# Optimization experiments

Measured on AMD Instinct MI355X. Metric: run time of the kernel, lower is better.

## Reference

```python
import jax, jax.numpy as jnp
import numpy as np

HIDDEN = 768
NUM_HEADS = 12
HEAD_SIZE = HIDDEN // NUM_HEADS
LN_EPS = 1e-5


def setup_inputs() -> dict:
    key = jax.random.key(0)
    ks = jax.random.split(key, 10)
    B, S, H = 2, 4096, HIDDEN
    std = 1.0 / np.sqrt(H)
    inp = {
        "hidden_states": jax.random.normal(ks[0], (B, S, H), dtype=jnp.float32),
        "attention_mask": jnp.ones((B, S), dtype=jnp.float32),
        "Wq": jax.random.normal(ks[1], (H, H), dtype=jnp.float32) * std,
        "bq": jnp.zeros((H,), dtype=jnp.float32),
        "Wk": jax.random.normal(ks[2], (H, H), dtype=jnp.float32) * std,
        "bk": jnp.zeros((H,), dtype=jnp.float32),
        "Wv": jax.random.normal(ks[3], (H, H), dtype=jnp.float32) * std,
        "bv": jnp.zeros((H,), dtype=jnp.float32),
        "Wo": jax.random.normal(ks[4], (H, H), dtype=jnp.float32) * std,
        "bo": jnp.zeros((H,), dtype=jnp.float32),
        "ln_gamma": jnp.ones((H,), dtype=jnp.float32),
        "ln_beta": jnp.zeros((H,), dtype=jnp.float32),
    }
    return inp


def _split_heads(x):
    # [B, S, H] -> [B, nH, S, hd]
    B, S, _ = x.shape
    return x.reshape(B, S, NUM_HEADS, HEAD_SIZE).transpose(0, 2, 1, 3)


def reference(hidden_states, attention_mask, Wq, bq, Wk, bk, Wv, bv, Wo, bo, ln_gamma, ln_beta):
    # QKV projections (torch Linear: x @ W.T + b; here W is stored as [in, out])
    q = _split_heads(hidden_states @ Wq + bq)
    k = _split_heads(hidden_states @ Wk + bk)
    v = _split_heads(hidden_states @ Wv + bv)

    scores = jnp.einsum("bhqd,bhkd->bhqk", q, k) / jnp.sqrt(jnp.float32(HEAD_SIZE))
    # additive mask: (1 - mask) * -10000, broadcast over heads and query positions
    scores = scores + (1.0 - attention_mask)[:, None, None, :] * -10000.0
    probs = jax.nn.softmax(scores, axis=-1)  # dropout_prob = 0 -> identity

    ctx = jnp.einsum("bhqk,bhkd->bhqd", probs, v)
    B, _, S, _ = ctx.shape
    ctx = ctx.transpose(0, 2, 1, 3).reshape(B, S, HIDDEN)

    out = ctx @ Wo + bo
    resid = out + hidden_states
    mu = jnp.mean(resid, axis=-1, keepdims=True)
    var = jnp.var(resid, axis=-1, keepdims=True)
    return (resid - mu) * jax.lax.rsqrt(var + LN_EPS) * ln_gamma + ln_beta
```

## Files before the change

### kernel.cpp

```cpp
#include <hip/hip_runtime.h>
#include <hip/hip_bf16.h>

#define HID 768
#define NHEADS 12
#define HDIM 64
#define SEQ 4096
#define BB 2
#define MTOT (BB * SEQ)

typedef __attribute__((ext_vector_type(8))) short bf16x8;
typedef __attribute__((ext_vector_type(16))) float f32x16;

#define LOG2E 1.4426950408889634f

__device__ inline unsigned pack2bf(float a, float b) {
    __hip_bfloat162 h = __float22bfloat162_rn(float2{a, b});
    return *(unsigned*)&h;
}

__global__ __launch_bounds__(256) void pack_w_kernel(
    const float* __restrict__ Wq, const float* __restrict__ Wk,
    const float* __restrict__ Wv, const float* __restrict__ Wo,
    __hip_bfloat16* __restrict__ Wt)
{
    const int z = blockIdx.z;
    const float* __restrict__ W = (z == 0) ? Wq : (z == 1) ? Wk : (z == 2) ? Wv : Wo;
    const int in0  = blockIdx.x * 64;
    const int out0 = blockIdx.y * 64;
    const int t = threadIdx.x;

    __shared__ float T[64][65];
#pragma unroll
    for (int i = 0; i < 4; ++i) {
        const int idx = t + 256 * i;
        const int row = idx >> 4;
        const int c4  = (idx & 15) << 2;
        const float4 v = *(const float4*)(W + (size_t)(in0 + row) * HID + out0 + c4);
        T[row][c4 + 0] = v.x; T[row][c4 + 1] = v.y;
        T[row][c4 + 2] = v.z; T[row][c4 + 3] = v.w;
    }
    __syncthreads();

    const int o  = t >> 2;
    const int cb = (t & 3) << 4;
    __hip_bfloat16 tmp[16];
#pragma unroll
    for (int k = 0; k < 16; ++k)
        tmp[k] = __float2bfloat16(T[cb + k][o]);
    __hip_bfloat16* __restrict__ dst =
        Wt + (size_t)(z * HID + out0 + o) * HID + in0 + cb;
    *(uint4*)(dst)     = *(uint4*)(&tmp[0]);
    *(uint4*)(dst + 8) = *(uint4*)(&tmp[8]);
}

__global__ __launch_bounds__(256) void qkv_mfma_kernel(
    const float* __restrict__ X, const __hip_bfloat16* __restrict__ Wt,
    const float* __restrict__ bq, const float* __restrict__ bk,
    const float* __restrict__ bv,
    __hip_bfloat16* __restrict__ Qo, __hip_bfloat16* __restrict__ Ko,
    __hip_bfloat16* __restrict__ Vo)
{
    const int nblk = blockIdx.x;
    const int z  = nblk / 6;
    const int f0 = (nblk % 6) * 128;
    const int n0 = nblk * 128;
    const int m0 = blockIdx.y * 128;

    const float* __restrict__ bias = (z == 0) ? bq : (z == 1) ? bk : bv;

    const int t    = threadIdx.x;
    const int w    = t >> 6;
    const int lane = t & 63;
    const int col  = lane & 31;
    const int g    = lane >> 5;
    const int wm   = w & 1;
    const int wn   = w >> 1;

    __shared__ __hip_bfloat16 smem[2 * 128 * 72];
    __hip_bfloat16 (*As)[72] = (__hip_bfloat16(*)[72])smem;
    __hip_bfloat16 (*Bs)[72] = (__hip_bfloat16(*)[72])(smem + 128 * 72);

    f32x16 acc[2][2];
#pragma unroll
    for (int mt = 0; mt < 2; ++mt)
#pragma unroll
        for (int nt = 0; nt < 2; ++nt)
#pragma unroll
            for (int r = 0; r < 16; ++r) acc[mt][nt][r] = 0.f;

    for (int k0 = 0; k0 < HID; k0 += 64) {
        __syncthreads();
#pragma unroll
        for (int i = 0; i < 4; ++i) {
            const int idx = t + 256 * i;
            const int row = idx >> 3;
            const int c8  = (idx & 7) << 3;
            const float* xp = X + (size_t)(m0 + row) * HID + k0 + c8;
            const float4 xa = *(const float4*)xp;
            const float4 xb = *(const float4*)(xp + 4);
            unsigned pu[4];
            pu[0] = pack2bf(xa.x, xa.y);
            pu[1] = pack2bf(xa.z, xa.w);
            pu[2] = pack2bf(xb.x, xb.y);
            pu[3] = pack2bf(xb.z, xb.w);
            *(uint4*)&As[row][c8] = *(uint4*)pu;
            *(uint4*)&Bs[row][c8] = *(const uint4*)(Wt + (size_t)(n0 + row) * HID + k0 + c8);
        }
        __syncthreads();
#pragma unroll
        for (int kh = 0; kh < 4; ++kh) {
            const int ko = 16 * kh + 8 * g;
            const bf16x8 a0 = *(const bf16x8*)&As[64 * wm + col][ko];
            const bf16x8 a1 = *(const bf16x8*)&As[64 * wm + 32 + col][ko];
            const bf16x8 b0 = *(const bf16x8*)&Bs[64 * wn + col][ko];
            const bf16x8 b1 = *(const bf16x8*)&Bs[64 * wn + 32 + col][ko];
            acc[0][0] = __builtin_amdgcn_mfma_f32_32x32x16_bf16(a0, b0, acc[0][0], 0, 0, 0);
            acc[0][1] = __builtin_amdgcn_mfma_f32_32x32x16_bf16(a0, b1, acc[0][1], 0, 0, 0);
            acc[1][0] = __builtin_amdgcn_mfma_f32_32x32x16_bf16(a1, b0, acc[1][0], 0, 0, 0);
            acc[1][1] = __builtin_amdgcn_mfma_f32_32x32x16_bf16(a1, b1, acc[1][1], 0, 0, 0);
        }
    }

    if (z < 2) {
        __hip_bfloat16* __restrict__ Out = (z == 0) ? Qo : Ko;
        const int h = (f0 >> 6) + wn;
#pragma unroll
        for (int mt = 0; mt < 2; ++mt)
#pragma unroll
            for (int nt = 0; nt < 2; ++nt) {
                const int d = 32 * nt + col;
                const float bsv = bias[f0 + 64 * wn + d];
#pragma unroll
                for (int r = 0; r < 16; ++r) {
                    const int m = m0 + 64 * wm + 32 * mt + (r & 3) + 8 * (r >> 2) + 4 * g;
                    const int b = m >> 12;
                    const int s = m & (SEQ - 1);
                    Out[(((size_t)(b * NHEADS + h)) * SEQ + s) * HDIM + d] =
                        __float2bfloat16(acc[mt][nt][r] + bsv);
                }
            }
    } else {
        __syncthreads();
        __hip_bfloat16 (*Ts)[136] = (__hip_bfloat16(*)[136])smem;
#pragma unroll
        for (int mt = 0; mt < 2; ++mt)
#pragma unroll
            for (int nt = 0; nt < 2; ++nt) {
                const int nloc = 64 * wn + 32 * nt + col;
                const float bsv = bias[f0 + nloc];
#pragma unroll
                for (int rg = 0; rg < 4; ++rg) {
                    const int mbase = 64 * wm + 32 * mt + 8 * rg + 4 * g;
                    unsigned pu[2];
                    pu[0] = pack2bf(acc[mt][nt][4 * rg + 0] + bsv,
                                    acc[mt][nt][4 * rg + 1] + bsv);
                    pu[1] = pack2bf(acc[mt][nt][4 * rg + 2] + bsv,
                                    acc[mt][nt][4 * rg + 3] + bsv);
                    *(uint2*)&Ts[nloc][mbase] = *(uint2*)pu;
                }
            }
        __syncthreads();
        const int nloc = t >> 1;
        const int half = t & 1;
        const int hh = (f0 >> 6) + (nloc >> 6);
        const int d  = nloc & 63;
        const int bb = m0 >> 12;
        const int s0 = m0 & (SEQ - 1);
        __hip_bfloat16* __restrict__ dst =
            Vo + (((size_t)(bb * NHEADS + hh)) * HDIM + d) * SEQ + s0 + 64 * half;
        const __hip_bfloat16* srcp = &Ts[nloc][64 * half];
#pragma unroll
        for (int j = 0; j < 8; ++j)
            *(uint4*)(dst + 8 * j) = *(const uint4*)(srcp + 8 * j);
    }
}

__global__ __launch_bounds__(256, 3) void attn_kernel(
    const __hip_bfloat16* __restrict__ Qb, const __hip_bfloat16* __restrict__ Kb,
    const __hip_bfloat16* __restrict__ Vt, const float* __restrict__ mask,
    __hip_bfloat16* __restrict__ Op, float* __restrict__ lp)
{
    const int bh = blockIdx.y;
    const int b  = bh / NHEADS;
    const int h  = bh - b * NHEADS;
    const int kspan = SEQ / gridDim.z;
    const int kbeg  = blockIdx.z * kspan;

    const int t    = threadIdx.x;
    const int w    = t >> 6;
    const int lane = t & 63;
    const int col  = lane & 31;
    const int g    = lane >> 5;
    const int qw   = blockIdx.x * 128 + 32 * w;

    __shared__ __hip_bfloat16 Ks[64][72];
    __shared__ __hip_bfloat16 Vts[64][72];
    __shared__ float madd[64];

    const __hip_bfloat16* __restrict__ Qh = Qb + (size_t)bh * SEQ * HDIM;
    const __hip_bfloat16* __restrict__ Kh = Kb + (size_t)bh * SEQ * HDIM;
    const __hip_bfloat16* __restrict__ Vh = Vt + (size_t)bh * HDIM * SEQ;

    bf16x8 bq[4];
#pragma unroll
    for (int kh = 0; kh < 4; ++kh)
        bq[kh] = *(const bf16x8*)(Qh + (size_t)(qw + col) * HDIM + 16 * kh + 8 * g);

    f32x16 O[2];
    float lac = 0.f;
#pragma unroll
    for (int dt = 0; dt < 2; ++dt)
#pragma unroll
        for (int r = 0; r < 16; ++r) O[dt][r] = 0.f;

    const float kscale = 0.125f * LOG2E;

    for (int kt0 = 0; kt0 < kspan; kt0 += 64) {
        const int kt = kbeg + kt0;
        __syncthreads();
#pragma unroll
        for (int i = 0; i < 2; ++i) {
            const int idx = t + 256 * i;
            const int row = idx >> 3;
            const int c8  = (idx & 7) << 3;
            *(uint4*)&Ks[row][c8]  = *(const uint4*)(Kh + (size_t)(kt + row) * HDIM + c8);
            *(uint4*)&Vts[row][c8] = *(const uint4*)(Vh + (size_t)row * SEQ + kt + c8);
        }
        if (t < 64) madd[t] = (1.0f - mask[b * SEQ + kt + t]) * (-10000.0f * LOG2E);
        __syncthreads();

        f32x16 St[2];
#pragma unroll
        for (int nt = 0; nt < 2; ++nt)
#pragma unroll
            for (int r = 0; r < 16; ++r) St[nt][r] = 0.f;

#pragma unroll
        for (int kh = 0; kh < 4; ++kh) {
            const bf16x8 ak0 = *(const bf16x8*)&Ks[col][16 * kh + 8 * g];
            const bf16x8 ak1 = *(const bf16x8*)&Ks[32 + col][16 * kh + 8 * g];
            St[0] = __builtin_amdgcn_mfma_f32_32x32x16_bf16(ak0, bq[kh], St[0], 0, 0, 0);
            St[1] = __builtin_amdgcn_mfma_f32_32x32x16_bf16(ak1, bq[kh], St[1], 0, 0, 0);
        }

        unsigned g4x[2][4], g4y[2][4];
#pragma unroll
        for (int nt = 0; nt < 2; ++nt) {
#pragma unroll
            for (int b4 = 0; b4 < 4; ++b4) {
                const float4 mm = *(const float4*)&madd[32 * nt + 8 * b4 + 4 * g];
                const float p0 = __builtin_amdgcn_exp2f(fmaf(St[nt][4 * b4 + 0], kscale, mm.x));
                const float p1 = __builtin_amdgcn_exp2f(fmaf(St[nt][4 * b4 + 1], kscale, mm.y));
                const float p2 = __builtin_amdgcn_exp2f(fmaf(St[nt][4 * b4 + 2], kscale, mm.z));
                const float p3 = __builtin_amdgcn_exp2f(fmaf(St[nt][4 * b4 + 3], kscale, mm.w));
                lac += (p0 + p1) + (p2 + p3);
                g4x[nt][b4] = pack2bf(p0, p1);
                g4y[nt][b4] = pack2bf(p2, p3);
            }
        }

#pragma unroll
        for (int kh = 0; kh < 4; ++kh) {
            const int nt  = kh >> 1;
            const int khl = kh & 1;
            const unsigned lo_x = g4x[nt][2 * khl],     lo_y = g4y[nt][2 * khl];
            const unsigned hi_x = g4x[nt][2 * khl + 1], hi_y = g4y[nt][2 * khl + 1];
            const unsigned sx = g ? lo_x : hi_x;
            const unsigned sy = g ? lo_y : hi_y;
            const unsigned rx = (unsigned)__shfl_xor((int)sx, 32, 64);
            const unsigned ry = (unsigned)__shfl_xor((int)sy, 32, 64);
            union { unsigned u[4]; bf16x8 v; } au;
            if (g) { au.u[0] = rx; au.u[1] = ry; au.u[2] = hi_x; au.u[3] = hi_y; }
            else   { au.u[0] = lo_x; au.u[1] = lo_y; au.u[2] = rx; au.u[3] = ry; }
            const bf16x8 bv0 = *(const bf16x8*)&Vts[col][16 * kh + 8 * g];
            const bf16x8 bv1 = *(const bf16x8*)&Vts[32 + col][16 * kh + 8 * g];
            O[0] = __builtin_amdgcn_mfma_f32_32x32x16_bf16(au.v, bv0, O[0], 0, 0, 0);
            O[1] = __builtin_amdgcn_mfma_f32_32x32x16_bf16(au.v, bv1, O[1], 0, 0, 0);
        }
    }

    const size_t opbase = (size_t)blockIdx.z * ((size_t)MTOT * HID);
    const float l = lac + __shfl_xor(lac, 32, 64);
    if (g == 0)
        lp[((size_t)blockIdx.z * (BB * NHEADS) + bh) * SEQ + qw + col] = l;
#pragma unroll
    for (int dt = 0; dt < 2; ++dt)
#pragma unroll
        for (int r = 0; r < 16; ++r) {
            const int q = qw + (r & 3) + 8 * (r >> 2) + 4 * g;
            const int d = 32 * dt + col;
            Op[opbase + ((size_t)b * SEQ + q) * HID + h * HDIM + d] =
                __float2bfloat16(O[dt][r]);
        }
}

__global__ __launch_bounds__(256) void combine_kernel(
    const __hip_bfloat16* __restrict__ Op, const float* __restrict__ lp,
    __hip_bfloat16* __restrict__ Ctx, int KS)
{
    const size_t i = ((size_t)blockIdx.x * 256 + threadIdx.x) * 8;
    const int n   = (int)(i % HID);
    const int row = (int)(i / HID);
    const int h = n >> 6;
    const int b = row >> 12;
    const int q = row & (SEQ - 1);
    const int bh = b * NHEADS + h;

    float denom = 0.f;
    float o[8] = {};
    for (int kz = 0; kz < KS; ++kz) {
        denom += lp[((size_t)kz * (BB * NHEADS) + bh) * SEQ + q];
        uint4 u = *(const uint4*)(Op + (size_t)kz * ((size_t)MTOT * HID) + i);
        const __hip_bfloat16* e = (const __hip_bfloat16*)&u;
#pragma unroll
        for (int j = 0; j < 8; ++j) o[j] += __bfloat162float(e[j]);
    }
    const float inv = 1.0f / denom;
    unsigned u[4];
#pragma unroll
    for (int j = 0; j < 4; ++j)
        u[j] = pack2bf(o[2 * j] * inv, o[2 * j + 1] * inv);
    *(uint4*)(Ctx + i) = *(uint4*)u;
}

__global__ __launch_bounds__(256) void out_mfma_kernel(
    const __hip_bfloat16* __restrict__ Cb, const __hip_bfloat16* __restrict__ Wto,
    const float* __restrict__ bo, const float* __restrict__ X,
    float* __restrict__ Resid)
{
    const int n0 = blockIdx.x * 128;
    const int m0 = blockIdx.y * 128;

    const int t    = threadIdx.x;
    const int w    = t >> 6;
    const int lane = t & 63;
    const int col  = lane & 31;
    const int g    = lane >> 5;
    const int wm   = w & 1;
    const int wn   = w >> 1;

    __shared__ __hip_bfloat16 As[128][72];
    __shared__ __hip_bfloat16 Bs[128][72];

    f32x16 acc[2][2];
#pragma unroll
    for (int mt = 0; mt < 2; ++mt)
#pragma unroll
        for (int nt = 0; nt < 2; ++nt)
#pragma unroll
            for (int r = 0; r < 16; ++r) acc[mt][nt][r] = 0.f;

    for (int k0 = 0; k0 < HID; k0 += 64) {
        __syncthreads();
#pragma unroll
        for (int i = 0; i < 4; ++i) {
            const int idx = t + 256 * i;
            const int row = idx >> 3;
            const int c8  = (idx & 7) << 3;
            *(uint4*)&As[row][c8] = *(const uint4*)(Cb  + (size_t)(m0 + row) * HID + k0 + c8);
            *(uint4*)&Bs[row][c8] = *(const uint4*)(Wto + (size_t)(n0 + row) * HID + k0 + c8);
        }
        __syncthreads();
#pragma unroll
        for (int kh = 0; kh < 4; ++kh) {
            const int ko = 16 * kh + 8 * g;
            const bf16x8 a0 = *(const bf16x8*)&As[64 * wm + col][ko];
            const bf16x8 a1 = *(const bf16x8*)&As[64 * wm + 32 + col][ko];
            const bf16x8 b0 = *(const bf16x8*)&Bs[64 * wn + col][ko];
            const bf16x8 b1 = *(const bf16x8*)&Bs[64 * wn + 32 + col][ko];
            acc[0][0] = __builtin_amdgcn_mfma_f32_32x32x16_bf16(a0, b0, acc[0][0], 0, 0, 0);
            acc[0][1] = __builtin_amdgcn_mfma_f32_32x32x16_bf16(a0, b1, acc[0][1], 0, 0, 0);
            acc[1][0] = __builtin_amdgcn_mfma_f32_32x32x16_bf16(a1, b0, acc[1][0], 0, 0, 0);
            acc[1][1] = __builtin_amdgcn_mfma_f32_32x32x16_bf16(a1, b1, acc[1][1], 0, 0, 0);
        }
    }

#pragma unroll
    for (int mt = 0; mt < 2; ++mt)
#pragma unroll
        for (int nt = 0; nt < 2; ++nt) {
            const int n = n0 + 64 * wn + 32 * nt + col;
            const float bsv = bo[n];
#pragma unroll
            for (int r = 0; r < 16; ++r) {
                const int m = m0 + 64 * wm + 32 * mt + (r & 3) + 8 * (r >> 2) + 4 * g;
                Resid[(size_t)m * HID + n] = acc[mt][nt][r] + bsv + X[(size_t)m * HID + n];
            }
        }
}

__global__ __launch_bounds__(256) void ln_kernel(
    const float* __restrict__ Rin, const float* __restrict__ gamma,
    const float* __restrict__ beta, float* __restrict__ Out)
{
    const int row = blockIdx.x;
    const int t   = threadIdx.x;
    const float* __restrict__ x = Rin + (size_t)row * HID;

    const float v0 = x[t];
    const float v1 = x[t + 256];
    const float v2 = x[t + 512];
    float s  = v0 + v1 + v2;
    float s2 = v0 * v0 + v1 * v1 + v2 * v2;
#pragma unroll
    for (int off = 32; off; off >>= 1) {
        s  += __shfl_xor(s,  off, 64);
        s2 += __shfl_xor(s2, off, 64);
    }
    __shared__ float rs[4], rs2[4];
    const int w = t >> 6, lane = t & 63;
    if (lane == 0) { rs[w] = s; rs2[w] = s2; }
    __syncthreads();
    const float tot  = rs[0] + rs[1] + rs[2] + rs[3];
    const float tot2 = rs2[0] + rs2[1] + rs2[2] + rs2[3];
    const float mu   = tot * (1.0f / HID);
    const float var  = tot2 * (1.0f / HID) - mu * mu;
    const float rsig = rsqrtf(var + 1e-5f);

    float* __restrict__ y = Out + (size_t)row * HID;
    y[t]       = (v0 - mu) * rsig * gamma[t]       + beta[t];
    y[t + 256] = (v1 - mu) * rsig * gamma[t + 256] + beta[t + 256];
    y[t + 512] = (v2 - mu) * rsig * gamma[t + 512] + beta[t + 512];
}

extern "C" void kernel_launch(void* const* d_in, const int* in_sizes, int n_in,
                              void* d_out, int out_size, void* d_ws, size_t ws_size,
                              hipStream_t stream)
{
    const float* X     = (const float*)d_in[0];
    const float* mask  = (const float*)d_in[1];
    const float* Wq    = (const float*)d_in[2];
    const float* bq    = (const float*)d_in[3];
    const float* Wk    = (const float*)d_in[4];
    const float* bk    = (const float*)d_in[5];
    const float* Wv    = (const float*)d_in[6];
    const float* bv    = (const float*)d_in[7];
    const float* Wo    = (const float*)d_in[8];
    const float* bo    = (const float*)d_in[9];
    const float* gamma = (const float*)d_in[10];
    const float* beta  = (const float*)d_in[11];
    float* out = (float*)d_out;

    const size_t N = (size_t)MTOT * HID;
    const size_t WTE = (size_t)4 * HID * HID;

    char* p = (char*)d_ws;
    __hip_bfloat16* Wt  = (__hip_bfloat16*)p;  p += 2 * WTE;
    __hip_bfloat16* Qw  = (__hip_bfloat16*)p;  p += 2 * N;
    __hip_bfloat16* Kw  = (__hip_bfloat16*)p;  p += 2 * N;
    __hip_bfloat16* Vtw = (__hip_bfloat16*)p;  p += 2 * N;
    char* opb = p;
    const size_t fixed = (size_t)(opb - (char*)d_ws);

    const size_t lpsz4 = 4 * (size_t)(BB * NHEADS) * SEQ * sizeof(float);
    const int KS = (ws_size >= fixed + 4 * 2 * N + lpsz4) ? 4 : 2;

    __hip_bfloat16* Op  = (__hip_bfloat16*)opb;
    float* lpt = (float*)(opb + (size_t)KS * 2 * N);
    __hip_bfloat16* Ctxb = Qw;
    float* Rd = (float*)Kw;

    pack_w_kernel<<<dim3(12, 12, 4), 256, 0, stream>>>(Wq, Wk, Wv, Wo, Wt);
    qkv_mfma_kernel<<<dim3(18, MTOT / 128), 256, 0, stream>>>(
        X, Wt, bq, bk, bv, Qw, Kw, Vtw);
    attn_kernel<<<dim3(SEQ / 128, BB * NHEADS, KS), 256, 0, stream>>>(
        Qw, Kw, Vtw, mask, Op, lpt);
    combine_kernel<<<(int)(N / 2048), 256, 0, stream>>>(Op, lpt, Ctxb, KS);
    out_mfma_kernel<<<dim3(6, MTOT / 128), 256, 0, stream>>>(
        Ctxb, Wt + (size_t)2304 * HID, bo, X, Rd);
    ln_kernel<<<MTOT, 256, 0, stream>>>(Rd, gamma, beta, out);
}
```

Measured before the change: 343.7 us.

## Pre-cast X to bf16 once and double the attention key tile

A new kernel converts the fp32 hidden states to bf16 once, so the QKV GEMM loads bf16 directly instead of re-converting each X tile for all 18 column blocks. The attention kernel now stages 128 keys per iteration, processed as two 64-key sub-tiles, which halves the barriers and loop overhead per key. It also seeds the first score MFMA with a zero accumulator. In exchange this adds a kernel launch, an extra activation-sized buffer in the workspace, and more shared memory per attention block, which may reduce occupancy.

```diff
diff --git a/kernel.cpp b/kernel.cpp
--- a/kernel.cpp
+++ b/kernel.cpp
@@ -16,6 +16,20 @@
 __device__ inline unsigned pack2bf(float a, float b) {
     __hip_bfloat162 h = __float22bfloat162_rn(float2{a, b});
     return *(unsigned*)&h;
+}
+
+__global__ __launch_bounds__(256) void cast_x_kernel(
+    const float* __restrict__ X, __hip_bfloat16* __restrict__ Xb)
+{
+    const size_t i = ((size_t)blockIdx.x * 256 + threadIdx.x) * 8;
+    const float4 x0 = *(const float4*)(X + i);
+    const float4 x1 = *(const float4*)(X + i + 4);
+    unsigned u[4];
+    u[0] = pack2bf(x0.x, x0.y);
+    u[1] = pack2bf(x0.z, x0.w);
+    u[2] = pack2bf(x1.x, x1.y);
+    u[3] = pack2bf(x1.z, x1.w);
+    *(uint4*)(Xb + i) = *(uint4*)u;
 }
 
 __global__ __launch_bounds__(256) void pack_w_kernel(
@@ -54,7 +68,7 @@
 }
 
 __global__ __launch_bounds__(256) void qkv_mfma_kernel(
-    const float* __restrict__ X, const __hip_bfloat16* __restrict__ Wt,
+    const __hip_bfloat16* __restrict__ Xb, const __hip_bfloat16* __restrict__ Wt,
     const float* __restrict__ bq, const float* __restrict__ bk,
     const float* __restrict__ bv,
     __hip_bfloat16* __restrict__ Qo, __hip_bfloat16* __restrict__ Ko,
@@ -95,15 +109,7 @@
             const int idx = t + 256 * i;
             const int row = idx >> 3;
             const int c8  = (idx & 7) << 3;
-            const float* xp = X + (size_t)(m0 + row) * HID + k0 + c8;
-            const float4 xa = *(const float4*)xp;
-            const float4 xb = *(const float4*)(xp + 4);
-            unsigned pu[4];
-            pu[0] = pack2bf(xa.x, xa.y);
-            pu[1] = pack2bf(xa.z, xa.w);
-            pu[2] = pack2bf(xb.x, xb.y);
-            pu[3] = pack2bf(xb.z, xb.w);
-            *(uint4*)&As[row][c8] = *(uint4*)pu;
+            *(uint4*)&As[row][c8] = *(const uint4*)(Xb + (size_t)(m0 + row) * HID + k0 + c8);
             *(uint4*)&Bs[row][c8] = *(const uint4*)(Wt + (size_t)(n0 + row) * HID + k0 + c8);
         }
         __syncthreads();
@@ -193,9 +199,9 @@
     const int g    = lane >> 5;
     const int qw   = blockIdx.x * 128 + 32 * w;
 
-    __shared__ __hip_bfloat16 Ks[64][72];
-    __shared__ __hip_bfloat16 Vts[64][72];
-    __shared__ float madd[64];
+    __shared__ __hip_bfloat16 Ks[128][72];
+    __shared__ __hip_bfloat16 Vts[64][136];
+    __shared__ float madd[128];
 
     const __hip_bfloat16* __restrict__ Qh = Qb + (size_t)bh * SEQ * HDIM;
     const __hip_bfloat16* __restrict__ Kh = Kb + (size_t)bh * SEQ * HDIM;
@@ -207,75 +213,82 @@
         bq[kh] = *(const bf16x8*)(Qh + (size_t)(qw + col) * HDIM + 16 * kh + 8 * g);
 
     f32x16 O[2];
+    f32x16 ZERO;
     float lac = 0.f;
 #pragma unroll
-    for (int dt = 0; dt < 2; ++dt)
-#pragma unroll
-        for (int r = 0; r < 16; ++r) O[dt][r] = 0.f;
+    for (int r = 0; r < 16; ++r) { O[0][r] = 0.f; O[1][r] = 0.f; ZERO[r] = 0.f; }
 
     const float kscale = 0.125f * LOG2E;
 
-    for (int kt0 = 0; kt0 < kspan; kt0 += 64) {
+    for (int kt0 = 0; kt0 < kspan; kt0 += 128) {
         const int kt = kbeg + kt0;
         __syncthreads();
 #pragma unroll
-        for (int i = 0; i < 2; ++i) {
+        for (int i = 0; i < 4; ++i) {
             const int idx = t + 256 * i;
-            const int row = idx >> 3;
-            const int c8  = (idx & 7) << 3;
-            *(uint4*)&Ks[row][c8]  = *(const uint4*)(Kh + (size_t)(kt + row) * HDIM + c8);
-            *(uint4*)&Vts[row][c8] = *(const uint4*)(Vh + (size_t)row * SEQ + kt + c8);
-        }
-        if (t < 64) madd[t] = (1.0f - mask[b * SEQ + kt + t]) * (-10000.0f * LOG2E);
-        __syncthreads();
-
-        f32x16 St[2];
-#pragma unroll
-        for (int nt = 0; nt < 2; ++nt)
-#pragma unroll
-            for (int r = 0; r < 16; ++r) St[nt][r] = 0.f;
-
-#pragma unroll
-        for (int kh = 0; kh < 4; ++kh) {
-            const bf16x8 ak0 = *(const bf16x8*)&Ks[col][16 * kh + 8 * g];
-            const bf16x8 ak1 = *(const bf16x8*)&Ks[32 + col][16 * kh + 8 * g];
-            St[0] = __builtin_amdgcn_mfma_f32_32x32x16_bf16(ak0, bq[kh], St[0], 0, 0, 0);
-            St[1] = __builtin_amdgcn_mfma_f32_32x32x16_bf16(ak1, bq[kh], St[1], 0, 0, 0);
-        }
-
-        unsigned g4x[2][4], g4y[2][4];
-#pragma unroll
-        for (int nt = 0; nt < 2; ++nt) {
-#pragma unroll
-            for (int b4 = 0; b4 < 4; ++b4) {
-                const float4 mm = *(const float4*)&madd[32 * nt + 8 * b4 + 4 * g];
-                const float p0 = __builtin_amdgcn_exp2f(fmaf(St[nt][4 * b4 + 0], kscale, mm.x));
-                const float p1 = __builtin_amdgcn_exp2f(fmaf(St[nt][4 * b4 + 1], kscale, mm.y));
-                const float p2 = __builtin_amdgcn_exp2f(fmaf(St[nt][4 * b4 + 2], kscale, mm.z));
-                const float p3 = __builtin_amdgcn_exp2f(fmaf(St[nt][4 * b4 + 3], kscale, mm.w));
-                lac += (p0 + p1) + (p2 + p3);
-                g4x[nt][b4] = pack2bf(p0, p1);
-                g4y[nt][b4] = pack2bf(p2, p3);
-            }
-        }
-
-#pragma unroll
-        for (int kh = 0; kh < 4; ++kh) {
-            const int nt  = kh >> 1;
-            const int khl = kh & 1;
-            const unsigned lo_x = g4x[nt][2 * khl],     lo_y = g4y[nt][2 * khl];
-            const unsigned hi_x = g4x[nt][2 * khl + 1], hi_y = g4y[nt][2 * khl + 1];
-            const unsigned sx = g ? lo_x : hi_x;
-            const unsigned sy = g ? lo_y : hi_y;
-            const unsigned rx = (unsigned)__shfl_xor((int)sx, 32, 64);
-            const unsigned ry = (unsigned)__shfl_xor((int)sy, 32, 64);
-            union { unsigned u[4]; bf16x8 v; } au;
-            if (g) { au.u[0] = rx; au.u[1] = ry; au.u[2] = hi_x; au.u[3] = hi_y; }
-            else   { au.u[0] = lo_x; au.u[1] = lo_y; au.u[2] = rx; au.u[3] = ry; }
-            const bf16x8 bv0 = *(const bf16x8*)&Vts[col][16 * kh + 8 * g];
-            const bf16x8 bv1 = *(const bf16x8*)&Vts[32 + col][16 * kh + 8 * g];
-            O[0] = __builtin_amdgcn_mfma_f32_32x32x16_bf16(au.v, bv0, O[0], 0, 0, 0);
-            O[1] = __builtin_amdgcn_mfma_f32_32x32x16_bf16(au.v, bv1, O[1], 0, 0, 0);
+            const int krow = idx >> 3;
+            const int kc8  = (idx & 7) << 3;
+            *(uint4*)&Ks[krow][kc8] = *(const uint4*)(Kh + (size_t)(kt + krow) * HDIM + kc8);
+            const int vrow = idx >> 4;
+            const int vc8  = (idx & 15) << 3;
+            *(uint4*)&Vts[vrow][vc8] = *(const uint4*)(Vh + (size_t)vrow * SEQ + kt + vc8);
+        }
+        if (t < 128) madd[t] = (1.0f - mask[b * SEQ + kt + t]) * (-10000.0f * LOG2E);
+        __syncthreads();
+
+#pragma unroll
+        for (int sub = 0; sub < 2; ++sub) {
+            const int kb = 64 * sub;
+
+            f32x16 St[2];
+            {
+                const bf16x8 ak0 = *(const bf16x8*)&Ks[kb + col][8 * g];
+                const bf16x8 ak1 = *(const bf16x8*)&Ks[kb + 32 + col][8 * g];
+                St[0] = __builtin_amdgcn_mfma_f32_32x32x16_bf16(ak0, bq[0], ZERO, 0, 0, 0);
+                St[1] = __builtin_amdgcn_mfma_f32_32x32x16_bf16(ak1, bq[0], ZERO, 0, 0, 0);
+            }
+#pragma unroll
+            for (int kh = 1; kh < 4; ++kh) {
+                const bf16x8 ak0 = *(const bf16x8*)&Ks[kb + col][16 * kh + 8 * g];
+                const bf16x8 ak1 = *(const bf16x8*)&Ks[kb + 32 + col][16 * kh + 8 * g];
+                St[0] = __builtin_amdgcn_mfma_f32_32x32x16_bf16(ak0, bq[kh], St[0], 0, 0, 0);
+                St[1] = __builtin_amdgcn_mfma_f32_32x32x16_bf16(ak1, bq[kh], St[1], 0, 0, 0);
+            }
+
+            unsigned g4x[2][4], g4y[2][4];
+#pragma unroll
+            for (int nt = 0; nt < 2; ++nt) {
+#pragma unroll
+                for (int b4 = 0; b4 < 4; ++b4) {
+                    const float4 mm = *(const float4*)&madd[kb + 32 * nt + 8 * b4 + 4 * g];
+                    const float p0 = __builtin_amdgcn_exp2f(fmaf(St[nt][4 * b4 + 0], kscale, mm.x));
+                    const float p1 = __builtin_amdgcn_exp2f(fmaf(St[nt][4 * b4 + 1], kscale, mm.y));
+                    const float p2 = __builtin_amdgcn_exp2f(fmaf(St[nt][4 * b4 + 2], kscale, mm.z));
+                    const float p3 = __builtin_amdgcn_exp2f(fmaf(St[nt][4 * b4 + 3], kscale, mm.w));
+                    lac += (p0 + p1) + (p2 + p3);
+                    g4x[nt][b4] = pack2bf(p0, p1);
+                    g4y[nt][b4] = pack2bf(p2, p3);
+                }
+            }
+
+#pragma unroll
+            for (int kh = 0; kh < 4; ++kh) {
+                const int nt  = kh >> 1;
+                const int khl = kh & 1;
+                const unsigned lo_x = g4x[nt][2 * khl],     lo_y = g4y[nt][2 * khl];
+                const unsigned hi_x = g4x[nt][2 * khl + 1], hi_y = g4y[nt][2 * khl + 1];
+                const unsigned sx = g ? lo_x : hi_x;
+                const unsigned sy = g ? lo_y : hi_y;
+                const unsigned rx = (unsigned)__shfl_xor((int)sx, 32, 64);
+                const unsigned ry = (unsigned)__shfl_xor((int)sy, 32, 64);
+                union { unsigned u[4]; bf16x8 v; } au;
+                if (g) { au.u[0] = rx; au.u[1] = ry; au.u[2] = hi_x; au.u[3] = hi_y; }
+                else   { au.u[0] = lo_x; au.u[1] = lo_y; au.u[2] = rx; au.u[3] = ry; }
+                const bf16x8 bv0 = *(const bf16x8*)&Vts[col][kb + 16 * kh + 8 * g];
+                const bf16x8 bv1 = *(const bf16x8*)&Vts[32 + col][kb + 16 * kh + 8 * g];
+                O[0] = __builtin_amdgcn_mfma_f32_32x32x16_bf16(au.v, bv0, O[0], 0, 0, 0);
+                O[1] = __builtin_amdgcn_mfma_f32_32x32x16_bf16(au.v, bv1, O[1], 0, 0, 0);
+            }
         }
     }
 
@@ -445,6 +458,7 @@
     const size_t WTE = (size_t)4 * HID * HID;
 
     char* p = (char*)d_ws;
+    __hip_bfloat16* Xb  = (__hip_bfloat16*)p;  p += 2 * N;
     __hip_bfloat16* Wt  = (__hip_bfloat16*)p;  p += 2 * WTE;
     __hip_bfloat16* Qw  = (__hip_bfloat16*)p;  p += 2 * N;
     __hip_bfloat16* Kw  = (__hip_bfloat16*)p;  p += 2 * N;
@@ -457,12 +471,13 @@
 
     __hip_bfloat16* Op  = (__hip_bfloat16*)opb;
     float* lpt = (float*)(opb + (size_t)KS * 2 * N);
-    __hip_bfloat16* Ctxb = Qw;
+    __hip_bfloat16* Ctxb = Xb;
     float* Rd = (float*)Kw;
 
+    cast_x_kernel<<<(int)(N / 2048), 256, 0, stream>>>(X, Xb);
     pack_w_kernel<<<dim3(12, 12, 4), 256, 0, stream>>>(Wq, Wk, Wv, Wo, Wt);
     qkv_mfma_kernel<<<dim3(18, MTOT / 128), 256, 0, stream>>>(
-        X, Wt, bq, bk, bv, Qw, Kw, Vtw);
+        Xb, Wt, bq, bk, bv, Qw, Kw, Vtw);
     attn_kernel<<<dim3(SEQ / 128, BB * NHEADS, KS), 256, 0, stream>>>(
         Qw, Kw, Vtw, mask, Op, lpt);
     combine_kernel<<<(int)(N / 2048), 256, 0, stream>>>(Op, lpt, Ctxb, KS);
```

Measured after the change: 337.8 us. About the same (-1.7%).
